# Kernel tuning notes

Hardware: AMD Instinct MI355X
Metric: run time of the kernel (lower is better)

## Reference

```python
import jax, jax.numpy as jnp
import numpy as np

D_K = 256

def setup_inputs() -> dict:
    key = jax.random.key(0)
    k1, k2, k3, k4 = jax.random.split(key, 4)
    B, S, D = 4, 4096, 256
    x = jax.random.normal(k1, (B, S, D), dtype=jnp.float32)
    scale = 1.0 / np.sqrt(D)
    W_q = jax.random.normal(k2, (D, D_K), dtype=jnp.float32) * scale
    W_k = jax.random.normal(k3, (D, D_K), dtype=jnp.float32) * scale
    W_v = jax.random.normal(k4, (D, D_K), dtype=jnp.float32) * scale
    return {"x": x, "W_q": W_q, "W_k": W_k, "W_v": W_v}

def reference(x, W_q, W_k, W_v):
    # x: [B, S, D]; weights: [D, d_k]
    B, S, D = x.shape
    Q = jnp.einsum('bsd,dk->bsk', x, W_q)
    K = jnp.einsum('bsd,dk->bsk', x, W_k)
    V = jnp.einsum('bsd,dk->bsk', x, W_v)
    scores = jnp.einsum('bqk,bsk->bqs', Q, K) / jnp.sqrt(jnp.float32(D_K))  # [B, S, S]
    causal = jnp.tril(jnp.ones((S, S), dtype=bool))
    scores = jnp.where(causal[None, :, :], scores, -jnp.inf)
    weights = jax.nn.softmax(scores, axis=-1)
    return jnp.einsum('bqs,bsk->bqk', weights, V)
```

## Files before the change

kernel.cpp:

```cpp
#include <hip/hip_runtime.h>
#include <hip/hip_bf16.h>
#include <cstdint>


typedef __bf16 b8v __attribute__((ext_vector_type(8)));
typedef __bf16 b4v __attribute__((ext_vector_type(4)));
typedef float  f4v __attribute__((ext_vector_type(4)));
typedef float  f16v __attribute__((ext_vector_type(16)));
typedef int    i4v __attribute__((ext_vector_type(4)));
typedef int    i2v __attribute__((ext_vector_type(2)));

#define MFMA16(a, b, c) __builtin_amdgcn_mfma_f32_16x16x32_bf16((a), (b), (c), 0, 0, 0)
#define MFMA32(a, b, c) __builtin_amdgcn_mfma_f32_32x32x16_bf16((a), (b), (c), 0, 0, 0)

#define GLOAD_LDS(gsrc, ldst)                                                        \
  __builtin_amdgcn_global_load_lds((const __attribute__((address_space(1))) void*)(gsrc), \
                                   (__attribute__((address_space(3))) void*)(ldst), 16, 0, 0)

#define SCALE_Q 0.09016844005f
#define MASKVAL -3.0e38f

static constexpr int DT = 20;

static constexpr size_t WS_WT = 0;
static constexpr size_t WS_Q  = 524288;
static constexpr size_t WS_K  = WS_Q + 8388608;
static constexpr size_t WS_VT = WS_K + 8388608;

__global__ void prep_wt(const float* __restrict__ Wq, const float* __restrict__ Wk,
                        const float* __restrict__ Wv, __bf16* __restrict__ wt) {
  int gid = blockIdx.x * blockDim.x + threadIdx.x;
  int w = gid >> 16, rem = gid & 65535;
  int c = rem >> 8, d = rem & 255;
  const float* W = (w == 0) ? Wq : (w == 1) ? Wk : Wv;
  float v = W[d * 256 + c];
  if (w == 0) v *= SCALE_Q;
  wt[gid] = (__bf16)v;
}

__global__ void __launch_bounds__(256, 2) proj_qkv(
    const float* __restrict__ x, const __bf16* __restrict__ wt,
    __bf16* __restrict__ Qw, __bf16* __restrict__ Kw, __bf16* __restrict__ Vt) {
  __shared__ __bf16 w_lds[16384];
  __shared__ __bf16 v_lds[64][72];
  const int tid = threadIdx.x;
  const int wv = tid >> 6, lane = tid & 63, c = lane & 15, g = lane >> 4;
  const int ww = blockIdx.x >> 8, rb = blockIdx.x & 255;
  const int rowbase = rb * 64;
  const int batch = rb >> 6, sblk = rb & 63;

  b8v xf[8];
  {
    const float* xr = x + (size_t)(rowbase + wv * 16 + c) * 256;
#pragma unroll
    for (int ks = 0; ks < 8; ++ks) {
      const float4 a0 = *reinterpret_cast<const float4*>(xr + 32 * ks + 8 * g);
      const float4 a1 = *reinterpret_cast<const float4*>(xr + 32 * ks + 8 * g + 4);
      b8v f;
      f[0] = (__bf16)a0.x; f[1] = (__bf16)a0.y; f[2] = (__bf16)a0.z; f[3] = (__bf16)a0.w;
      f[4] = (__bf16)a1.x; f[5] = (__bf16)a1.y; f[6] = (__bf16)a1.z; f[7] = (__bf16)a1.w;
      xf[ks] = f;
    }
  }
  const __bf16* wbase = wt + (size_t)ww * 65536;
  char* wl = reinterpret_cast<char*>(w_lds);
  for (int ct = 0; ct < 4; ++ct) {
    __syncthreads();
    {
#pragma unroll
      for (int i = 0; i < 8; ++i) {
        const int n = i * 256 + tid;
        const int r = n >> 5, cp = n & 31;
        const __bf16* src = wbase + (size_t)(ct * 64 + r) * 256 + ((cp ^ (r & 7)) << 3);
        GLOAD_LDS(src, wl + ((i * 256 + wv * 64) << 4));
      }
    }
    __syncthreads();
    f4v pacc[4];
#pragma unroll
    for (int i = 0; i < 4; ++i) pacc[i] = (f4v){0.f, 0.f, 0.f, 0.f};
#pragma unroll
    for (int ks = 0; ks < 8; ++ks) {
#pragma unroll
      for (int nf = 0; nf < 4; ++nf) {
        const b8v wf = *reinterpret_cast<const b8v*>(
            wl + (16 * nf + c) * 512 + (((4 * ks + g) ^ (c & 7)) << 4));
        pacc[nf] = MFMA16(xf[ks], wf, pacc[nf]);
      }
    }
    if (ww < 2) {
      __bf16* o = (ww == 0) ? Qw : Kw;
      const int row0 = rowbase + wv * 16 + 4 * g;
#pragma unroll
      for (int nf = 0; nf < 4; ++nf) {
        const int col = ct * 64 + 16 * nf + c;
#pragma unroll
        for (int r = 0; r < 4; ++r)
          o[(size_t)(row0 + r) * 256 + col] = (__bf16)pacc[nf][r];
      }
    } else {
      const int sp = 16 * wv + 4 * g;
#pragma unroll
      for (int nf = 0; nf < 4; ++nf) {
        b4v pk;
        pk[0] = (__bf16)pacc[nf][0]; pk[1] = (__bf16)pacc[nf][1];
        pk[2] = (__bf16)pacc[nf][2]; pk[3] = (__bf16)pacc[nf][3];
        *reinterpret_cast<b4v*>(&v_lds[16 * nf + c][sp]) = pk;
      }
      __syncthreads();
      {
        const int dd = tid >> 2, ch = tid & 3;
        const b8v* sp8 = reinterpret_cast<const b8v*>(&v_lds[dd][ch * 16]);
        __bf16* dst =
            Vt + ((size_t)(batch * 256 + ct * 64 + dd)) * 4096 + sblk * 64 + ch * 16;
        reinterpret_cast<b8v*>(dst)[0] = sp8[0];
        reinterpret_cast<b8v*>(dst)[1] = sp8[1];
      }
    }
  }
}

__global__ void __launch_bounds__(512, 2) attn_fwd(
    const __bf16* __restrict__ Qw, const __bf16* __restrict__ Kw,
    const __bf16* __restrict__ Vt, float* __restrict__ out,
    float* __restrict__ lsum_buf, int CB) {
  extern __shared__ char smem[];
  const int tid = threadIdx.x;
  const int wv = tid >> 6, lane = tid & 63;
  const int q5 = lane & 31, hi = lane >> 5;

  const int p = blockIdx.x;
  const int bb = p & 3;
  const int slot = p >> 2;
  if (slot >= CB) return;

  int Q = 0, acc0 = 0, c = 1;
  for (; Q < 16; ++Q) {
    const int T_ = 8 * Q + 8;
    c = (T_ + DT - 1) / DT;
    if (acc0 + c > slot) break;
    acc0 += c;
  }
  const int j = slot - acc0;
  const int T = 8 * Q + 8;
  const int ta = j * T / c, tb = (j + 1) * T / c;
  const bool single = (c == 1);

  const __bf16* Kg = Kw + (size_t)bb * 4096 * 256;
  const __bf16* Vg = Vt + (size_t)bb * 256 * 4096;

  auto stage = [&](int sb, int tt) {
    char* Kd = smem + sb * 32768;
    char* Vd = Kd + 16384;
#pragma unroll
    for (int i = 0; i < 2; ++i) {
      const int n = i * 512 + tid;
      const int r = n >> 5, cp = n & 31;
      const __bf16* src = Kg + (size_t)(tt * 32 + r) * 256 + ((cp ^ r) << 3);
      GLOAD_LDS(src, Kd + ((i * 512 + wv * 64) << 4));
    }
#pragma unroll
    for (int i = 0; i < 2; ++i) {
      const int n = i * 512 + tid;
      const int d = n >> 2, cp = n & 3;
      const __bf16* src =
          Vg + (size_t)d * 4096 + tt * 32 + ((cp ^ ((d >> 3) & 3)) << 3);
      GLOAD_LDS(src, Vd + ((i * 512 + wv * 64) << 4));
    }
  };

  b8v qf[16];
  {
    const __bf16* qr =
        Qw + ((size_t)(bb * 4096 + Q * 256 + wv * 32 + q5)) * 256 + 8 * hi;
#pragma unroll
    for (int ks = 0; ks < 16; ++ks)
      qf[ks] = *reinterpret_cast<const b8v*>(qr + ks * 16);
  }

  f16v acc[8];
#pragma unroll
  for (int i = 0; i < 8; ++i)
#pragma unroll
    for (int jj = 0; jj < 16; ++jj) acc[i][jj] = 0.f;
  float lsum = 0.f;
  const int qg = Q * 256 + wv * 32 + q5;

  stage(0, ta);
  __syncthreads();

  for (int tt = ta; tt < tb; ++tt) {
    const int cur = (tt - ta) & 1;
    if (tt + 1 < tb) stage(cur ^ 1, tt + 1);

    f16v sv;
#pragma unroll
    for (int jj = 0; jj < 16; ++jj) sv[jj] = 0.f;
    const char* kb0 = smem + cur * 32768 + q5 * 512;
    __builtin_amdgcn_s_setprio(1);
#pragma unroll
    for (int ks = 0; ks < 16; ++ks) {
      const int co = (((ks << 1) | hi) ^ q5) << 4;
      const b8v k0 = *reinterpret_cast<const b8v*>(kb0 + co);
      sv = MFMA32(k0, qf[ks], sv);
    }
    __builtin_amdgcn_s_setprio(0);

    if (tt * 32 + 31 > Q * 256 + wv * 32) {
#pragma unroll
      for (int reg = 0; reg < 16; ++reg) {
        const int R = (reg & 3) + 8 * (reg >> 2) + 4 * hi;
        if (tt * 32 + R > qg) sv[reg] = MASKVAL;
      }
    }
#pragma unroll
    for (int jj = 0; jj < 16; ++jj) sv[jj] = exp2f(sv[jj]);
    {
      float u0 = 0.f, u1s = 0.f, u2 = 0.f, u3 = 0.f;
#pragma unroll
      for (int jj = 0; jj < 16; jj += 4) {
        u0 += sv[jj]; u1s += sv[jj + 1]; u2 += sv[jj + 2]; u3 += sv[jj + 3];
      }
      lsum += (u0 + u1s) + (u2 + u3);
    }
    unsigned a0[4], a1[4];
#pragma unroll
    for (int mb = 0; mb < 4; ++mb) {
      b4v pk;
      pk[0] = (__bf16)sv[4 * mb]; pk[1] = (__bf16)sv[4 * mb + 1];
      pk[2] = (__bf16)sv[4 * mb + 2]; pk[3] = (__bf16)sv[4 * mb + 3];
      const uint2 uu = *reinterpret_cast<uint2*>(&pk);
      a0[mb] = uu.x; a1[mb] = uu.y;
    }
    const char* vbase = smem + cur * 32768 + 16384 + q5 * 64;
#pragma unroll
    for (int ks = 0; ks < 2; ++ks) {
      i4v wi;
#if __has_builtin(__builtin_amdgcn_permlane32_swap)
      const i2v e0 = __builtin_amdgcn_permlane32_swap((int)a0[2 * ks],
                                                      (int)a0[2 * ks + 1], false, false);
      const i2v e1 = __builtin_amdgcn_permlane32_swap((int)a1[2 * ks],
                                                      (int)a1[2 * ks + 1], false, false);
      wi[0] = e0[0]; wi[1] = e1[0]; wi[2] = e0[1]; wi[3] = e1[1];
#else
      const unsigned x0 = (unsigned)__shfl_xor((int)a0[2 * ks], 32);
      const unsigned x1 = (unsigned)__shfl_xor((int)a1[2 * ks], 32);
      const unsigned y0 = (unsigned)__shfl_xor((int)a0[2 * ks + 1], 32);
      const unsigned y1 = (unsigned)__shfl_xor((int)a1[2 * ks + 1], 32);
      wi[0] = hi ? (int)y0 : (int)a0[2 * ks];
      wi[1] = hi ? (int)y1 : (int)a1[2 * ks];
      wi[2] = hi ? (int)a0[2 * ks + 1] : (int)x0;
      wi[3] = hi ? (int)a1[2 * ks + 1] : (int)x1;
#endif
      const b8v pa = *reinterpret_cast<b8v*>(&wi);
      const int cov = ((((ks << 1) | hi)) ^ ((q5 >> 3) & 3)) << 4;
      __builtin_amdgcn_s_setprio(1);
#pragma unroll
      for (int db = 0; db < 8; ++db) {
        const b8v vf = *reinterpret_cast<const b8v*>(vbase + db * 2048 + cov);
        acc[db] = MFMA32(pa, vf, acc[db]);
      }
      __builtin_amdgcn_s_setprio(0);
    }
    __syncthreads();
  }

  lsum += __shfl_xor(lsum, 32);
  if (single) {
    const float inv = 1.f / lsum;
#pragma unroll
    for (int reg = 0; reg < 16; ++reg) {
      const int R = (reg & 3) + 8 * (reg >> 2) + 4 * hi;
      const float ivr = __shfl(inv, R);
      float* orow = out + ((size_t)(bb * 4096 + Q * 256 + wv * 32 + R)) * 256 + q5;
#pragma unroll
      for (int db = 0; db < 8; ++db) orow[db * 32] = acc[db][reg] * ivr;
    }
  } else {
#pragma unroll
    for (int reg = 0; reg < 16; ++reg) {
      const int R = (reg & 3) + 8 * (reg >> 2) + 4 * hi;
      float* orow = out + ((size_t)(bb * 4096 + Q * 256 + wv * 32 + R)) * 256 + q5;
#pragma unroll
      for (int db = 0; db < 8; ++db) atomicAdd(&orow[db * 32], acc[db][reg]);
    }
    if (hi == 0)
      atomicAdd(&lsum_buf[(size_t)bb * 4096 + Q * 256 + wv * 32 + q5], lsum);
  }
}

__global__ void __launch_bounds__(256) combine_k(float* __restrict__ out,
                                                 const float* __restrict__ lsum_buf) {
  const int row = blockIdx.x * 32 + (threadIdx.x >> 3);
  const int Q = (row >> 8) & 15;
  if (8 * Q + 8 <= DT) return;
  const float inv = 1.f / lsum_buf[row];
  float* dst = out + (size_t)row * 256 + (threadIdx.x & 7) * 32;
#pragma unroll
  for (int k = 0; k < 8; ++k) {
    f4v v = reinterpret_cast<const f4v*>(dst)[k];
    reinterpret_cast<f4v*>(dst)[k] = v * inv;
  }
}

extern "C" void kernel_launch(void* const* d_in, const int* in_sizes, int n_in,
                              void* d_out, int out_size, void* d_ws, size_t ws_size,
                              hipStream_t stream) {
  const float* x  = reinterpret_cast<const float*>(d_in[0]);
  const float* Wq = reinterpret_cast<const float*>(d_in[1]);
  const float* Wk = reinterpret_cast<const float*>(d_in[2]);
  const float* Wv = reinterpret_cast<const float*>(d_in[3]);
  char* ws = reinterpret_cast<char*>(d_ws);
  __bf16* wt = reinterpret_cast<__bf16*>(ws + WS_WT);
  __bf16* Qw = reinterpret_cast<__bf16*>(ws + WS_Q);
  __bf16* Kw = reinterpret_cast<__bf16*>(ws + WS_K);
  __bf16* Vt = reinterpret_cast<__bf16*>(ws + WS_VT);
  float* lsum_buf = reinterpret_cast<float*>(ws);
  float* out = reinterpret_cast<float*>(d_out);

  int CB = 0;
  for (int Q = 0; Q < 16; ++Q) CB += (8 * Q + 8 + DT - 1) / DT;

  for (int b = 0; b < 4; ++b)
    (void)hipMemsetAsync(out + ((size_t)b * 4096 + 512) * 256, 0,
                         (size_t)3584 * 256 * 4, stream);
  prep_wt<<<768, 256, 0, stream>>>(Wq, Wk, Wv, wt);
  proj_qkv<<<768, 256, 0, stream>>>(x, wt, Qw, Kw, Vt);
  (void)hipMemsetAsync(lsum_buf, 0, 4 * 4096 * sizeof(float), stream);

  constexpr int kSmem = 65536;
  (void)hipFuncSetAttribute(reinterpret_cast<const void*>(attn_fwd),
                            hipFuncAttributeMaxDynamicSharedMemorySize, kSmem);
  attn_fwd<<<4 * 64, 512, kSmem, stream>>>(Qw, Kw, Vt, out, lsum_buf, CB);
  combine_k<<<512, 256, 0, stream>>>(out, lsum_buf);
}
```

Measured before the change: 139.1 us.

## Fold memsets into prep kernel and compute all three projections per block

Removes the five hipMemsetAsync calls by having prep_wt zero the output regions and the lsum buffer. The lsum buffer moves to its own workspace offset so it no longer aliases the weight area. proj_qkv now launches 256 blocks, each looping over Q, K and V, so x is loaded and converted to bf16 once instead of three times. In exchange the projection has fewer blocks, which lowers parallelism on a large GPU, and each block runs three times as many serial steps.

```diff
diff --git a/kernel.cpp b/kernel.cpp
--- a/kernel.cpp
+++ b/kernel.cpp
@@ -22,20 +22,35 @@
 
 static constexpr int DT = 20;
 
-static constexpr size_t WS_WT = 0;
-static constexpr size_t WS_Q  = 524288;
-static constexpr size_t WS_K  = WS_Q + 8388608;
-static constexpr size_t WS_VT = WS_K + 8388608;
+static constexpr size_t WS_WT   = 0;
+static constexpr size_t WS_LSUM = 393216;
+static constexpr size_t WS_Q    = 524288;
+static constexpr size_t WS_K    = WS_Q + 8388608;
+static constexpr size_t WS_VT   = WS_K + 8388608;
 
 __global__ void prep_wt(const float* __restrict__ Wq, const float* __restrict__ Wk,
-                        const float* __restrict__ Wv, __bf16* __restrict__ wt) {
-  int gid = blockIdx.x * blockDim.x + threadIdx.x;
-  int w = gid >> 16, rem = gid & 65535;
-  int c = rem >> 8, d = rem & 255;
-  const float* W = (w == 0) ? Wq : (w == 1) ? Wk : Wv;
-  float v = W[d * 256 + c];
-  if (w == 0) v *= SCALE_Q;
-  wt[gid] = (__bf16)v;
+                        const float* __restrict__ Wv, __bf16* __restrict__ wt,
+                        float* __restrict__ out, float* __restrict__ lsum_buf) {
+  const int gid = blockIdx.x * blockDim.x + threadIdx.x;
+  {
+    int w = gid >> 16, rem = gid & 65535;
+    int c = rem >> 8, d = rem & 255;
+    const float* W = (w == 0) ? Wq : (w == 1) ? Wk : Wv;
+    float v = W[d * 256 + c];
+    if (w == 0) v *= SCALE_Q;
+    wt[gid] = (__bf16)v;
+  }
+  if (gid < 16384) lsum_buf[gid] = 0.f;
+  const f4v z = {0.f, 0.f, 0.f, 0.f};
+#pragma unroll
+  for (int k = 0; k < 5; ++k) {
+    const int idx = k * 196608 + gid;
+    if (idx < 917504) {
+      const int b = idx / 229376;
+      const int r = idx - b * 229376;
+      *reinterpret_cast<f4v*>(out + ((size_t)(b * 4096 + 512)) * 256 + (size_t)r * 4) = z;
+    }
+  }
 }
 
 __global__ void __launch_bounds__(256, 2) proj_qkv(
@@ -45,7 +60,7 @@
   __shared__ __bf16 v_lds[64][72];
   const int tid = threadIdx.x;
   const int wv = tid >> 6, lane = tid & 63, c = lane & 15, g = lane >> 4;
-  const int ww = blockIdx.x >> 8, rb = blockIdx.x & 255;
+  const int rb = blockIdx.x;
   const int rowbase = rb * 64;
   const int batch = rb >> 6, sblk = rb & 63;
 
@@ -62,59 +77,62 @@
       xf[ks] = f;
     }
   }
-  const __bf16* wbase = wt + (size_t)ww * 65536;
   char* wl = reinterpret_cast<char*>(w_lds);
-  for (int ct = 0; ct < 4; ++ct) {
-    __syncthreads();
-    {
-#pragma unroll
-      for (int i = 0; i < 8; ++i) {
-        const int n = i * 256 + tid;
-        const int r = n >> 5, cp = n & 31;
-        const __bf16* src = wbase + (size_t)(ct * 64 + r) * 256 + ((cp ^ (r & 7)) << 3);
-        GLOAD_LDS(src, wl + ((i * 256 + wv * 64) << 4));
-      }
-    }
-    __syncthreads();
-    f4v pacc[4];
-#pragma unroll
-    for (int i = 0; i < 4; ++i) pacc[i] = (f4v){0.f, 0.f, 0.f, 0.f};
-#pragma unroll
-    for (int ks = 0; ks < 8; ++ks) {
-#pragma unroll
-      for (int nf = 0; nf < 4; ++nf) {
-        const b8v wf = *reinterpret_cast<const b8v*>(
-            wl + (16 * nf + c) * 512 + (((4 * ks + g) ^ (c & 7)) << 4));
-        pacc[nf] = MFMA16(xf[ks], wf, pacc[nf]);
-      }
-    }
-    if (ww < 2) {
-      __bf16* o = (ww == 0) ? Qw : Kw;
-      const int row0 = rowbase + wv * 16 + 4 * g;
-#pragma unroll
-      for (int nf = 0; nf < 4; ++nf) {
-        const int col = ct * 64 + 16 * nf + c;
-#pragma unroll
-        for (int r = 0; r < 4; ++r)
-          o[(size_t)(row0 + r) * 256 + col] = (__bf16)pacc[nf][r];
-      }
-    } else {
-      const int sp = 16 * wv + 4 * g;
-#pragma unroll
-      for (int nf = 0; nf < 4; ++nf) {
-        b4v pk;
-        pk[0] = (__bf16)pacc[nf][0]; pk[1] = (__bf16)pacc[nf][1];
-        pk[2] = (__bf16)pacc[nf][2]; pk[3] = (__bf16)pacc[nf][3];
-        *reinterpret_cast<b4v*>(&v_lds[16 * nf + c][sp]) = pk;
-      }
+  for (int ww = 0; ww < 3; ++ww) {
+    const __bf16* wbase = wt + (size_t)ww * 65536;
+    for (int ct = 0; ct < 4; ++ct) {
       __syncthreads();
       {
-        const int dd = tid >> 2, ch = tid & 3;
-        const b8v* sp8 = reinterpret_cast<const b8v*>(&v_lds[dd][ch * 16]);
-        __bf16* dst =
-            Vt + ((size_t)(batch * 256 + ct * 64 + dd)) * 4096 + sblk * 64 + ch * 16;
-        reinterpret_cast<b8v*>(dst)[0] = sp8[0];
-        reinterpret_cast<b8v*>(dst)[1] = sp8[1];
+#pragma unroll
+        for (int i = 0; i < 8; ++i) {
+          const int n = i * 256 + tid;
+          const int r = n >> 5, cp = n & 31;
+          const __bf16* src =
+              wbase + (size_t)(ct * 64 + r) * 256 + ((cp ^ (r & 7)) << 3);
+          GLOAD_LDS(src, wl + ((i * 256 + wv * 64) << 4));
+        }
+      }
+      __syncthreads();
+      f4v pacc[4];
+#pragma unroll
+      for (int i = 0; i < 4; ++i) pacc[i] = (f4v){0.f, 0.f, 0.f, 0.f};
+#pragma unroll
+      for (int ks = 0; ks < 8; ++ks) {
+#pragma unroll
+        for (int nf = 0; nf < 4; ++nf) {
+          const b8v wf = *reinterpret_cast<const b8v*>(
+              wl + (16 * nf + c) * 512 + (((4 * ks + g) ^ (c & 7)) << 4));
+          pacc[nf] = MFMA16(xf[ks], wf, pacc[nf]);
+        }
+      }
+      if (ww < 2) {
+        __bf16* o = (ww == 0) ? Qw : Kw;
+        const int row0 = rowbase + wv * 16 + 4 * g;
+#pragma unroll
+        for (int nf = 0; nf < 4; ++nf) {
+          const int col = ct * 64 + 16 * nf + c;
+#pragma unroll
+          for (int r = 0; r < 4; ++r)
+            o[(size_t)(row0 + r) * 256 + col] = (__bf16)pacc[nf][r];
+        }
+      } else {
+        const int sp = 16 * wv + 4 * g;
+#pragma unroll
+        for (int nf = 0; nf < 4; ++nf) {
+          b4v pk;
+          pk[0] = (__bf16)pacc[nf][0]; pk[1] = (__bf16)pacc[nf][1];
+          pk[2] = (__bf16)pacc[nf][2]; pk[3] = (__bf16)pacc[nf][3];
+          *reinterpret_cast<b4v*>(&v_lds[16 * nf + c][sp]) = pk;
+        }
+        __syncthreads();
+        {
+          const int dd = tid >> 2, ch = tid & 3;
+          const b8v* sp8 = reinterpret_cast<const b8v*>(&v_lds[dd][ch * 16]);
+          __bf16* dst =
+              Vt + ((size_t)(batch * 256 + ct * 64 + dd)) * 4096 + sblk * 64 + ch * 16;
+          reinterpret_cast<b8v*>(dst)[0] = sp8[0];
+          reinterpret_cast<b8v*>(dst)[1] = sp8[1];
+        }
       }
     }
   }
@@ -315,18 +333,14 @@
   __bf16* Qw = reinterpret_cast<__bf16*>(ws + WS_Q);
   __bf16* Kw = reinterpret_cast<__bf16*>(ws + WS_K);
   __bf16* Vt = reinterpret_cast<__bf16*>(ws + WS_VT);
-  float* lsum_buf = reinterpret_cast<float*>(ws);
+  float* lsum_buf = reinterpret_cast<float*>(ws + WS_LSUM);
   float* out = reinterpret_cast<float*>(d_out);
 
   int CB = 0;
   for (int Q = 0; Q < 16; ++Q) CB += (8 * Q + 8 + DT - 1) / DT;
 
-  for (int b = 0; b < 4; ++b)
-    (void)hipMemsetAsync(out + ((size_t)b * 4096 + 512) * 256, 0,
-                         (size_t)3584 * 256 * 4, stream);
-  prep_wt<<<768, 256, 0, stream>>>(Wq, Wk, Wv, wt);
-  proj_qkv<<<768, 256, 0, stream>>>(x, wt, Qw, Kw, Vt);
-  (void)hipMemsetAsync(lsum_buf, 0, 4 * 4096 * sizeof(float), stream);
+  prep_wt<<<768, 256, 0, stream>>>(Wq, Wk, Wv, wt, out, lsum_buf);
+  proj_qkv<<<256, 256, 0, stream>>>(x, wt, Qw, Kw, Vt);
 
   constexpr int kSmem = 65536;
   (void)hipFuncSetAttribute(reinterpret_cast<const void*>(attn_fwd),
```

Measured after the change: 132.0 us. -5.1%, faster.
